# Optimization experiments

Hardware: AMD Instinct MI355X
Metric: run time of the kernel (lower is better)

## Reference

```python
import jax, jax.numpy as jnp
import numpy as np

M, N, DIM, B = 32000, 2048, 1024, 2048  # vocab, hidden, embed dim, batch
SIGMA = 20.0


def setup_inputs() -> dict:
    key = jax.random.key(0)
    ks = jax.random.split(key, 16)
    u = lambda k, shape: jax.random.uniform(k, shape, dtype=jnp.float32)
    return {
        "input_text": jax.random.randint(ks[0], (B,), 0, M),
        "h_prev": jax.random.normal(ks[1], (N, B), dtype=jnp.float32),
        "C_prev": jax.random.normal(ks[2], (N, B), dtype=jnp.float32),
        "emb": jax.random.normal(ks[3], (M, DIM), dtype=jnp.float32),
        "W_A": u(ks[4], (M, N)) / SIGMA,
        "W_C": u(ks[5], (N, N + DIM)) / SIGMA,
        "W_f": u(ks[6], (N, N + DIM)) / SIGMA,
        "W_o": u(ks[7], (N, N + DIM)) / SIGMA,
        "W_i": u(ks[8], (N, N + DIM)) / SIGMA,
        "b_A": u(ks[9], (M, 1)),
        "b_C": u(ks[10], (N, 1)),
        "b_f": u(ks[11], (N, 1)),
        "b_o": u(ks[12], (N, 1)),
        "b_i": u(ks[13], (N, 1)),
    }


def reference(input_text, h_prev, C_prev, emb, W_A, W_C, W_f, W_o, W_i,
              b_A, b_C, b_f, b_o, b_i):
    x = emb[input_text].T                     # [dim, B]
    z = jnp.concatenate([h_prev, x], axis=0)  # [n+dim, B]
    f = jax.nn.sigmoid(W_f @ z + b_f)
    i = jax.nn.sigmoid(W_i @ z + b_i)
    o = jax.nn.sigmoid(W_o @ z + b_o)
    tildeC = jnp.tanh(W_C @ z + b_C)
    C = f * C_prev + i * tildeC
    h = o * jnp.tanh(C)
    y = W_A @ h + b_A                         # [m, B]
    return (y, h, C)
```

## Files before the change

### kernel.cpp

```cpp
#include <hip/hip_runtime.h>

#define DM 32000
#define DN 2048
#define DD 1024
#define DB 2048
#define DKG 3072

typedef __attribute__((ext_vector_type(4))) float floatx4;
typedef __attribute__((ext_vector_type(8))) short shortx8;
typedef __attribute__((ext_vector_type(4))) short shortx4;

__device__ inline unsigned int f2bf(float f) {
    unsigned int u = __builtin_bit_cast(unsigned int, f);
    u += 0x7fffu + ((u >> 16) & 1u);
    return u >> 16;
}

__device__ inline float fast_sigmoid(float x) { return 1.0f / (1.0f + __expf(-x)); }
__device__ inline float fast_tanh(float x) { return 1.0f - 2.0f / (__expf(2.0f * x) + 1.0f); }

__global__ __launch_bounds__(256) void transpose_h_kernel(
    const float* __restrict__ h_prev, unsigned short* __restrict__ z_t)
{
    __shared__ unsigned short T[64 * 66];
    int t = threadIdx.x;
    int b0 = blockIdx.x * 64, k0 = blockIdx.y * 64;
    int bi = t & 63, wv = t >> 6;
    #pragma unroll
    for (int i = 0; i < 16; i++) {
        int kl = wv + i * 4;
        float v = h_prev[(size_t)(k0 + kl) * DB + b0 + bi];
        T[kl * 66 + bi] = (unsigned short)f2bf(v);
    }
    __syncthreads();
    #pragma unroll
    for (int i = 0; i < 16; i++) {
        int r = wv + i * 4;
        z_t[(size_t)(b0 + r) * DKG + k0 + bi] = T[bi * 66 + r];
    }
}

__global__ __launch_bounds__(256) void emb_gather_kernel(
    const int* __restrict__ idx, const float* __restrict__ emb,
    unsigned short* __restrict__ z_t)
{
    int b = blockIdx.x;
    int row = idx[b];
    int t = threadIdx.x;
    const floatx4 v = *(const floatx4*)(&emb[(size_t)row * DD + t * 4]);
    unsigned int p0 = (f2bf(v[1]) << 16) | f2bf(v[0]);
    unsigned int p1 = (f2bf(v[3]) << 16) | f2bf(v[2]);
    *(uint2*)(&z_t[(size_t)b * DKG + DN + t * 4]) = make_uint2(p0, p1);
}

#define BM 128
#define BN 128
#define BK 32
#define LS 40

__global__ __launch_bounds__(256, 3) void gemm_bt_kernel(
    const float* __restrict__ A0, const float* __restrict__ A1,
    const float* __restrict__ A2, const float* __restrict__ A3,
    const unsigned short* __restrict__ Bt,
    float* __restrict__ C0, float* __restrict__ C1,
    float* __restrict__ C2, float* __restrict__ C3,
    const float* __restrict__ bias, int K)
{
    __shared__ unsigned short As[BM * LS];
    __shared__ unsigned short Bs[BN * LS];
    int t = threadIdx.x;
    int lane = t & 63, wave = t >> 6;
    int wm = (wave >> 1) * 64, wn = (wave & 1) * 64;
    int zz = blockIdx.z;
    const float* A   = (zz == 0) ? A0 : (zz == 1) ? A1 : (zz == 2) ? A2 : A3;
    float*       Cout = (zz == 0) ? C0 : (zz == 1) ? C1 : (zz == 2) ? C2 : C3;
    size_t m0 = (size_t)blockIdx.y * BM, n0 = (size_t)blockIdx.x * BN;

    floatx4 acc[4][4] = {};

    int sa_row = t >> 3;
    int sa_col = (t & 7) * 4;
    int sb_row = t >> 2;
    int sb_col = (t & 3) * 8;
    int mrow = lane & 15;
    int koff = (lane >> 4) * 8;

    for (int k0 = 0; k0 < K; k0 += BK) {
        #pragma unroll
        for (int i = 0; i < 4; i++) {
            int row = i * 32 + sa_row;
            const floatx4 v = *(const floatx4*)(&A[(m0 + row) * (size_t)K + k0 + sa_col]);
            unsigned int p0 = (f2bf(v[1]) << 16) | f2bf(v[0]);
            unsigned int p1 = (f2bf(v[3]) << 16) | f2bf(v[2]);
            *(uint2*)(&As[row * LS + sa_col]) = make_uint2(p0, p1);
        }
        #pragma unroll
        for (int i = 0; i < 2; i++) {
            int row = i * 64 + sb_row;
            *(uint4*)(&Bs[row * LS + sb_col]) =
                *(const uint4*)(&Bt[(n0 + row) * (size_t)K + k0 + sb_col]);
        }
        __syncthreads();

        shortx8 af[4], bfv[4];
        #pragma unroll
        for (int mi = 0; mi < 4; mi++) {
            int o = (wm + mi * 16 + mrow) * LS + koff;
            shortx4 lo = *(const shortx4*)(&As[o]);
            shortx4 hi = *(const shortx4*)(&As[o + 4]);
            af[mi] = __builtin_shufflevector(lo, hi, 0, 1, 2, 3, 4, 5, 6, 7);
        }
        #pragma unroll
        for (int ni = 0; ni < 4; ni++) {
            int o = (wn + ni * 16 + mrow) * LS + koff;
            shortx4 lo = *(const shortx4*)(&Bs[o]);
            shortx4 hi = *(const shortx4*)(&Bs[o + 4]);
            bfv[ni] = __builtin_shufflevector(lo, hi, 0, 1, 2, 3, 4, 5, 6, 7);
        }
        #pragma unroll
        for (int mi = 0; mi < 4; mi++)
            #pragma unroll
            for (int ni = 0; ni < 4; ni++)
                acc[mi][ni] = __builtin_amdgcn_mfma_f32_16x16x32_bf16(
                    af[mi], bfv[ni], acc[mi][ni], 0, 0, 0);
        __syncthreads();
    }

    int cn = lane & 15;
    int rb = (lane >> 4) * 4;
    #pragma unroll
    for (int mi = 0; mi < 4; mi++) {
        #pragma unroll
        for (int r = 0; r < 4; r++) {
            size_t row = m0 + wm + mi * 16 + rb + r;
            float bv = bias ? bias[row] : 0.0f;
            #pragma unroll
            for (int ni = 0; ni < 4; ni++) {
                Cout[row * DB + n0 + wn + ni * 16 + cn] = acc[mi][ni][r] + bv;
            }
        }
    }
}

__global__ __launch_bounds__(256) void pointwise_kernel(
    const float* __restrict__ Pf, const float* __restrict__ Pi,
    const float* __restrict__ Po, const float* __restrict__ Pc,
    const float* __restrict__ C_prev,
    const float* __restrict__ b_f, const float* __restrict__ b_i,
    const float* __restrict__ b_o, const float* __restrict__ b_C,
    float* __restrict__ outH, float* __restrict__ outC,
    unsigned short* __restrict__ h_t)
{
    __shared__ unsigned short T[64 * 66];
    int t = threadIdx.x;
    int b0 = blockIdx.x * 64, n0 = blockIdx.y * 64;
    int bi = t & 63, wv = t >> 6;
    #pragma unroll
    for (int i = 0; i < 16; i++) {
        int nl = wv + i * 4;
        size_t idx = (size_t)(n0 + nl) * DB + b0 + bi;
        float f  = fast_sigmoid(Pf[idx] + b_f[n0 + nl]);
        float ii = fast_sigmoid(Pi[idx] + b_i[n0 + nl]);
        float o  = fast_sigmoid(Po[idx] + b_o[n0 + nl]);
        float tc = fast_tanh(Pc[idx] + b_C[n0 + nl]);
        float C  = f * C_prev[idx] + ii * tc;
        float h  = o * fast_tanh(C);
        outC[idx] = C;
        outH[idx] = h;
        T[nl * 66 + bi] = (unsigned short)f2bf(h);
    }
    __syncthreads();
    #pragma unroll
    for (int i = 0; i < 16; i++) {
        int r = wv + i * 4;
        h_t[(size_t)(b0 + r) * DN + n0 + bi] = T[bi * 66 + r];
    }
}

extern "C" void kernel_launch(void* const* d_in, const int* in_sizes, int n_in,
                              void* d_out, int out_size, void* d_ws, size_t ws_size,
                              hipStream_t stream)
{
    const int*   input_text = (const int*)d_in[0];
    const float* h_prev = (const float*)d_in[1];
    const float* C_prev = (const float*)d_in[2];
    const float* emb    = (const float*)d_in[3];
    const float* W_A    = (const float*)d_in[4];
    const float* W_C    = (const float*)d_in[5];
    const float* W_f    = (const float*)d_in[6];
    const float* W_o    = (const float*)d_in[7];
    const float* W_i    = (const float*)d_in[8];
    const float* b_A    = (const float*)d_in[9];
    const float* b_C    = (const float*)d_in[10];
    const float* b_f    = (const float*)d_in[11];
    const float* b_o    = (const float*)d_in[12];
    const float* b_i    = (const float*)d_in[13];

    char* ws = (char*)d_ws;
    unsigned short* z_t = (unsigned short*)ws;
    float* Pf = (float*)(ws + 12582912);
    float* Pi = (float*)(ws + 12582912 + 1 * 16777216);
    float* Po = (float*)(ws + 12582912 + 2 * 16777216);
    float* Pc = (float*)(ws + 12582912 + 3 * 16777216);
    unsigned short* h_t = (unsigned short*)(ws + 12582912 + 4 * 16777216);

    float* y    = (float*)d_out;
    float* outH = y + (size_t)DM * DB;
    float* outC = outH + (size_t)DN * DB;

    transpose_h_kernel<<<dim3(32, 32), 256, 0, stream>>>(h_prev, z_t);
    emb_gather_kernel<<<dim3(2048), 256, 0, stream>>>(input_text, emb, z_t);

    gemm_bt_kernel<<<dim3(16, 16, 4), 256, 0, stream>>>(
        W_f, W_i, W_o, W_C, z_t, Pf, Pi, Po, Pc, nullptr, DKG);

    pointwise_kernel<<<dim3(32, 32), 256, 0, stream>>>(
        Pf, Pi, Po, Pc, C_prev, b_f, b_i, b_o, b_C, outH, outC, h_t);

    gemm_bt_kernel<<<dim3(16, 250, 1), 256, 0, stream>>>(
        W_A, W_A, W_A, W_A, h_t, y, y, y, y, b_A, DN);
}
```

Baseline: 1.177 ms.

## Pre-convert W_A to bf16 and use direct-to-LDS loads with swizzled 64-wide K tiles

```diff
diff --git a/kernel.cpp b/kernel.cpp
--- a/kernel.cpp
+++ b/kernel.cpp
@@ -8,7 +8,6 @@
 
 typedef __attribute__((ext_vector_type(4))) float floatx4;
 typedef __attribute__((ext_vector_type(8))) short shortx8;
-typedef __attribute__((ext_vector_type(4))) short shortx4;
 
 __device__ inline unsigned int f2bf(float f) {
     unsigned int u = __builtin_bit_cast(unsigned int, f);
@@ -16,6 +15,19 @@
     return u >> 16;
 }
 
+__device__ inline unsigned int cvt_pk_bf16(float lo, float hi) {
+    unsigned int r;
+    asm("v_cvt_pk_bf16_f32 %0, %1, %2" : "=v"(r) : "v"(lo), "v"(hi));
+    return r;
+}
+
+__device__ inline void gld_lds16(const void* g, void* l) {
+    __builtin_amdgcn_global_load_lds(
+        (const __attribute__((address_space(1))) unsigned int*)g,
+        (__attribute__((address_space(3))) unsigned int*)l,
+        16, 0, 0);
+}
+
 __device__ inline float fast_sigmoid(float x) { return 1.0f / (1.0f + __expf(-x)); }
 __device__ inline float fast_tanh(float x) { return 1.0f - 2.0f / (__expf(2.0f * x) + 1.0f); }
 
@@ -53,91 +65,155 @@
     *(uint2*)(&z_t[(size_t)b * DKG + DN + t * 4]) = make_uint2(p0, p1);
 }
 
-#define BM 128
-#define BN 128
-#define BK 32
-#define LS 40
-
-__global__ __launch_bounds__(256, 3) void gemm_bt_kernel(
+__global__ __launch_bounds__(256) void wconv_kernel(
+    const float* __restrict__ src, unsigned short* __restrict__ dst)
+{
+    size_t i = ((size_t)blockIdx.x * 256 + threadIdx.x) * 8;
+    floatx4 v0 = *(const floatx4*)(src + i);
+    floatx4 v1 = *(const floatx4*)(src + i + 4);
+    uint4 p;
+    p.x = cvt_pk_bf16(v0[0], v0[1]);
+    p.y = cvt_pk_bf16(v0[2], v0[3]);
+    p.z = cvt_pk_bf16(v1[0], v1[1]);
+    p.w = cvt_pk_bf16(v1[2], v1[3]);
+    *(uint4*)(dst + i) = p;
+}
+
+
+__global__ __launch_bounds__(256, 3) void gemm_wa_kernel(
+    const unsigned short* __restrict__ A, const unsigned short* __restrict__ Bt,
+    float* __restrict__ C, const float* __restrict__ bias)
+{
+    __shared__ unsigned short As[128 * 64];
+    __shared__ unsigned short Bs[128 * 64];
+    const int K = DN;
+    int t = threadIdx.x;
+    int lane = t & 63, wave = t >> 6;
+    int wm = (wave >> 1) * 64, wn = (wave & 1) * 64;
+    size_t m0 = (size_t)blockIdx.y * 128, n0 = (size_t)blockIdx.x * 128;
+    int mrow = lane & 15, kgrp = lane >> 4, l7 = lane & 7;
+    int r8 = t >> 3, lsl = t & 7;
+    int ss = lsl ^ (r8 & 7);
+
+    floatx4 acc[4][4] = {};
+
+    for (int k0 = 0; k0 < K; k0 += 64) {
+        #pragma unroll
+        for (int i = 0; i < 4; i++) {
+            int row = i * 32 + r8;
+            gld_lds16(A  + (m0 + row) * (size_t)K + k0 + ss * 8,
+                      &As[(i * 256 + wave * 64) * 8]);
+            gld_lds16(Bt + (n0 + row) * (size_t)K + k0 + ss * 8,
+                      &Bs[(i * 256 + wave * 64) * 8]);
+        }
+        __syncthreads();
+        #pragma unroll
+        for (int ks = 0; ks < 2; ks++) {
+            int so = ((ks * 4 + kgrp) ^ l7) * 8;
+            shortx8 af[4], bfv[4];
+            #pragma unroll
+            for (int mi = 0; mi < 4; mi++)
+                af[mi] = *(const shortx8*)(&As[(wm + mi * 16 + mrow) * 64 + so]);
+            #pragma unroll
+            for (int ni = 0; ni < 4; ni++)
+                bfv[ni] = *(const shortx8*)(&Bs[(wn + ni * 16 + mrow) * 64 + so]);
+            #pragma unroll
+            for (int mi = 0; mi < 4; mi++)
+                #pragma unroll
+                for (int ni = 0; ni < 4; ni++)
+                    acc[mi][ni] = __builtin_amdgcn_mfma_f32_16x16x32_bf16(
+                        af[mi], bfv[ni], acc[mi][ni], 0, 0, 0);
+        }
+        __syncthreads();
+    }
+
+    int cn = lane & 15, rb = kgrp * 4;
+    #pragma unroll
+    for (int mi = 0; mi < 4; mi++) {
+        #pragma unroll
+        for (int r = 0; r < 4; r++) {
+            size_t row = m0 + wm + mi * 16 + rb + r;
+            float bv = bias[row];
+            #pragma unroll
+            for (int ni = 0; ni < 4; ni++)
+                C[row * DB + n0 + wn + ni * 16 + cn] = acc[mi][ni][r] + bv;
+        }
+    }
+}
+
+__global__ __launch_bounds__(256, 3) void gemm_gates_kernel(
     const float* __restrict__ A0, const float* __restrict__ A1,
     const float* __restrict__ A2, const float* __restrict__ A3,
     const unsigned short* __restrict__ Bt,
     float* __restrict__ C0, float* __restrict__ C1,
-    float* __restrict__ C2, float* __restrict__ C3,
-    const float* __restrict__ bias, int K)
-{
-    __shared__ unsigned short As[BM * LS];
-    __shared__ unsigned short Bs[BN * LS];
+    float* __restrict__ C2, float* __restrict__ C3)
+{
+    __shared__ unsigned short As[128 * 64];
+    __shared__ unsigned short Bs[128 * 64];
+    const int K = DKG;
     int t = threadIdx.x;
     int lane = t & 63, wave = t >> 6;
     int wm = (wave >> 1) * 64, wn = (wave & 1) * 64;
     int zz = blockIdx.z;
-    const float* A   = (zz == 0) ? A0 : (zz == 1) ? A1 : (zz == 2) ? A2 : A3;
-    float*       Cout = (zz == 0) ? C0 : (zz == 1) ? C1 : (zz == 2) ? C2 : C3;
-    size_t m0 = (size_t)blockIdx.y * BM, n0 = (size_t)blockIdx.x * BN;
+    const float* A = (zz == 0) ? A0 : (zz == 1) ? A1 : (zz == 2) ? A2 : A3;
+    float* Cout    = (zz == 0) ? C0 : (zz == 1) ? C1 : (zz == 2) ? C2 : C3;
+    size_t m0 = (size_t)blockIdx.y * 128, n0 = (size_t)blockIdx.x * 128;
+    int mrow = lane & 15, kgrp = lane >> 4, l7 = lane & 7;
+    int r8 = t >> 3, lsl = t & 7;
+    int ss = lsl ^ (r8 & 7);
 
     floatx4 acc[4][4] = {};
 
-    int sa_row = t >> 3;
-    int sa_col = (t & 7) * 4;
-    int sb_row = t >> 2;
-    int sb_col = (t & 3) * 8;
-    int mrow = lane & 15;
-    int koff = (lane >> 4) * 8;
-
-    for (int k0 = 0; k0 < K; k0 += BK) {
+    for (int k0 = 0; k0 < K; k0 += 64) {
         #pragma unroll
         for (int i = 0; i < 4; i++) {
-            int row = i * 32 + sa_row;
-            const floatx4 v = *(const floatx4*)(&A[(m0 + row) * (size_t)K + k0 + sa_col]);
-            unsigned int p0 = (f2bf(v[1]) << 16) | f2bf(v[0]);
-            unsigned int p1 = (f2bf(v[3]) << 16) | f2bf(v[2]);
-            *(uint2*)(&As[row * LS + sa_col]) = make_uint2(p0, p1);
-        }
-        #pragma unroll
-        for (int i = 0; i < 2; i++) {
-            int row = i * 64 + sb_row;
-            *(uint4*)(&Bs[row * LS + sb_col]) =
-                *(const uint4*)(&Bt[(n0 + row) * (size_t)K + k0 + sb_col]);
+            int row = i * 32 + r8;
+            gld_lds16(Bt + (n0 + row) * (size_t)K + k0 + ss * 8,
+                      &Bs[(i * 256 + wave * 64) * 8]);
+        }
+        #pragma unroll
+        for (int i = 0; i < 4; i++) {
+            int row = i * 32 + r8;
+            const float* src = A + (m0 + row) * (size_t)K + k0 + lsl * 8;
+            floatx4 v0 = *(const floatx4*)(src);
+            floatx4 v1 = *(const floatx4*)(src + 4);
+            uint4 p;
+            p.x = cvt_pk_bf16(v0[0], v0[1]);
+            p.y = cvt_pk_bf16(v0[2], v0[3]);
+            p.z = cvt_pk_bf16(v1[0], v1[1]);
+            p.w = cvt_pk_bf16(v1[2], v1[3]);
+            *(uint4*)(&As[(row * 8 + ss) * 8]) = p;
         }
         __syncthreads();
-
-        shortx8 af[4], bfv[4];
-        #pragma unroll
-        for (int mi = 0; mi < 4; mi++) {
-            int o = (wm + mi * 16 + mrow) * LS + koff;
-            shortx4 lo = *(const shortx4*)(&As[o]);
-            shortx4 hi = *(const shortx4*)(&As[o + 4]);
-            af[mi] = __builtin_shufflevector(lo, hi, 0, 1, 2, 3, 4, 5, 6, 7);
-        }
-        #pragma unroll
-        for (int ni = 0; ni < 4; ni++) {
-            int o = (wn + ni * 16 + mrow) * LS + koff;
-            shortx4 lo = *(const shortx4*)(&Bs[o]);
-            shortx4 hi = *(const shortx4*)(&Bs[o + 4]);
-            bfv[ni] = __builtin_shufflevector(lo, hi, 0, 1, 2, 3, 4, 5, 6, 7);
-        }
-        #pragma unroll
-        for (int mi = 0; mi < 4; mi++)
+        #pragma unroll
+        for (int ks = 0; ks < 2; ks++) {
+            int so = ((ks * 4 + kgrp) ^ l7) * 8;
+            shortx8 af[4], bfv[4];
+            #pragma unroll
+            for (int mi = 0; mi < 4; mi++)
+                af[mi] = *(const shortx8*)(&As[(wm + mi * 16 + mrow) * 64 + so]);
             #pragma unroll
             for (int ni = 0; ni < 4; ni++)
-                acc[mi][ni] = __builtin_amdgcn_mfma_f32_16x16x32_bf16(
-                    af[mi], bfv[ni], acc[mi][ni], 0, 0, 0);
+                bfv[ni] = *(const shortx8*)(&Bs[(wn + ni * 16 + mrow) * 64 + so]);
+            #pragma unroll
+            for (int mi = 0; mi < 4; mi++)
+                #pragma unroll
+                for (int ni = 0; ni < 4; ni++)
+                    acc[mi][ni] = __builtin_amdgcn_mfma_f32_16x16x32_bf16(
+                        af[mi], bfv[ni], acc[mi][ni], 0, 0, 0);
+        }
         __syncthreads();
     }
 
-    int cn = lane & 15;
-    int rb = (lane >> 4) * 4;
+    int cn = lane & 15, rb = kgrp * 4;
     #pragma unroll
     for (int mi = 0; mi < 4; mi++) {
         #pragma unroll
         for (int r = 0; r < 4; r++) {
             size_t row = m0 + wm + mi * 16 + rb + r;
-            float bv = bias ? bias[row] : 0.0f;
-            #pragma unroll
-            for (int ni = 0; ni < 4; ni++) {
-                Cout[row * DB + n0 + wn + ni * 16 + cn] = acc[mi][ni][r] + bv;
-            }
+            #pragma unroll
+            for (int ni = 0; ni < 4; ni++)
+                Cout[row * DB + n0 + wn + ni * 16 + cn] = acc[mi][ni][r];
         }
     }
 }
@@ -203,6 +279,7 @@
     float* Po = (float*)(ws + 12582912 + 2 * 16777216);
     float* Pc = (float*)(ws + 12582912 + 3 * 16777216);
     unsigned short* h_t = (unsigned short*)(ws + 12582912 + 4 * 16777216);
+    unsigned short* wa  = (unsigned short*)ws;
 
     float* y    = (float*)d_out;
     float* outH = y + (size_t)DM * DB;
@@ -211,12 +288,15 @@
     transpose_h_kernel<<<dim3(32, 32), 256, 0, stream>>>(h_prev, z_t);
     emb_gather_kernel<<<dim3(2048), 256, 0, stream>>>(input_text, emb, z_t);
 
-    gemm_bt_kernel<<<dim3(16, 16, 4), 256, 0, stream>>>(
-        W_f, W_i, W_o, W_C, z_t, Pf, Pi, Po, Pc, nullptr, DKG);
+    gemm_gates_kernel<<<dim3(16, 16, 4), 256, 0, stream>>>(
+        W_f, W_i, W_o, W_C, z_t, Pf, Pi, Po, Pc);
 
     pointwise_kernel<<<dim3(32, 32), 256, 0, stream>>>(
         Pf, Pi, Po, Pc, C_prev, b_f, b_i, b_o, b_C, outH, outC, h_t);
 
-    gemm_bt_kernel<<<dim3(16, 250, 1), 256, 0, stream>>>(
-        W_A, W_A, W_A, W_A, h_t, y, y, y, y, b_A, DN);
-}
+    wconv_kernel<<<dim3(16000), 256, 0, stream>>>(W_A, wa);
+    gemm_wa_kernel<<<dim3(16, 125), 256, 0, stream>>>(wa, h_t, y, b_A);
+    wconv_kernel<<<dim3(16000), 256, 0, stream>>>(W_A + (size_t)16000 * DN, wa);
+    gemm_wa_kernel<<<dim3(16, 125), 256, 0, stream>>>(
+        wa, h_t, y + (size_t)16000 * DB, b_A + 16000);
+}
```

After: 1.023 ms. -13.1%, faster.
